# Kernel tuning notes

Measured on AMD Instinct MI355X. Metric: run time of the kernel, lower is better.

## Reference

```python
import jax, jax.numpy as jnp
import numpy as np

N_NODES = 100000
N_EDGES = 1600000
FEAT_DIM = 128
EMBED_DIM = 32
N_CLASS_P1 = 17  # num_class + 1


def setup_inputs() -> dict:
    key = jax.random.key(0)
    ks = jax.random.split(key, 6)
    features = jax.random.normal(ks[0], (N_NODES, FEAT_DIM), dtype=jnp.float32)
    edges = jax.random.randint(ks[1], (N_EDGES, 2), 0, N_NODES, dtype=jnp.int64)
    weights = jax.random.uniform(ks[2], (N_EDGES,), dtype=jnp.float32)
    neighbours_sum = jax.random.uniform(ks[3], (N_NODES, 1), dtype=jnp.float32)
    W_embed = jax.random.normal(ks[4], (FEAT_DIM, EMBED_DIM), dtype=jnp.float32) / np.sqrt(FEAT_DIM)
    b_embed = jnp.zeros((EMBED_DIM,), dtype=jnp.float32)
    W_trans = jax.random.normal(ks[5], (2 * EMBED_DIM, N_CLASS_P1), dtype=jnp.float32) / np.sqrt(2 * EMBED_DIM)
    b_trans = jnp.zeros((N_CLASS_P1,), dtype=jnp.float32)
    return {
        "features": features, "edges": edges, "weights": weights,
        "neighbours_sum": neighbours_sum, "W_embed": W_embed, "b_embed": b_embed,
        "W_trans": W_trans, "b_trans": b_trans,
    }


def reference(features, edges, weights, neighbours_sum, W_embed, b_embed, W_trans, b_trans):
    num_nodes = features.shape[0]
    # node embedding: Linear(feature_dim -> num_dims)
    embed = features @ W_embed + b_embed               # [N, D]
    src_e = embed[edges[:, 0]]                         # [E, D] gather
    dst_e = embed[edges[:, 1]]                         # [E, D] gather
    # operator_sy1: [(src+dst)/2, (src-dst)^2]
    E_feat = jnp.concatenate([(src_e + dst_e) * 0.5, (src_e - dst_e) ** 2], axis=1)  # [E, 2D]
    poss_edge = jax.nn.softmax(E_feat @ W_trans + b_trans, axis=1)  # [E, C+1]
    # weighted scatter-add into nodes via edges[:,0]
    value = poss_edge * weights[:, None]
    recall_node = jax.ops.segment_sum(value, edges[:, 0], num_segments=num_nodes)  # [N, C+1]
    poss_node = recall_node / neighbours_sum
    return poss_node, poss_edge, recall_node
```

## Files before the change

kernel.cpp:

```cpp
#include <hip/hip_runtime.h>

#define NNODES 100000
#define NEDGES 1600000
#define FDIM 128
#define EDIM 32
#define NCLS 17
#define ROWU 16
#define BCAP 64
#define WPK (16 * NCLS)

typedef unsigned int u32;
typedef _Float16 h2 __attribute__((ext_vector_type(2)));

__device__ inline h2 bch(u32 x) { return __builtin_bit_cast(h2, x); }

__device__ inline float dot2acc(h2 a, u32 wbits, float acc) {
#if __has_builtin(__builtin_amdgcn_fdot2)
  return __builtin_amdgcn_fdot2(a, bch(wbits), acc, false);
#else
  h2 w = bch(wbits);
  acc = fmaf((float)a[0], (float)w[0], acc);
  return fmaf((float)a[1], (float)w[1], acc);
#endif
}

__global__ __launch_bounds__(256) void prep_kernel(
    const float* __restrict__ W_trans, u32* __restrict__ wpack)
{
  for (int x = threadIdx.x; x < 2 * WPK; x += 256) {
    int tab = x / WPK;
    int r   = x - tab * WPK;
    int k2  = r / NCLS, c = r - k2 * NCLS;
    int row0 = tab ? (EDIM + 2 * k2) : (2 * k2);
    float a = W_trans[row0 * NCLS + c];
    float b = W_trans[(row0 + 1) * NCLS + c];
    if (!tab) { a *= 0.5f; b *= 0.5f; }
    h2 p; p[0] = (_Float16)a; p[1] = (_Float16)b;
    wpack[x] = __builtin_bit_cast(u32, p);
  }
}

__global__ __launch_bounds__(64) void node_kernel(
    const float* __restrict__ features,
    const float* __restrict__ W_embed,
    const float* __restrict__ b_embed,
    u32* __restrict__ nodetab)
{
  int n = blockIdx.x * 64 + threadIdx.x;
  if (n >= NNODES) return;

  float acc[EDIM];
  #pragma unroll
  for (int c = 0; c < EDIM; ++c) acc[c] = b_embed[c];

  const float4* f4 = (const float4*)(features + (size_t)n * FDIM);
  for (int k4 = 0; k4 < FDIM / 4; ++k4) {
    float4 f = f4[k4];
    const float* w = W_embed + k4 * 4 * EDIM;
    #pragma unroll
    for (int c = 0; c < EDIM; ++c) {
      acc[c] = fmaf(f.x, w[c],            acc[c]);
      acc[c] = fmaf(f.y, w[EDIM + c],     acc[c]);
      acc[c] = fmaf(f.z, w[2 * EDIM + c], acc[c]);
      acc[c] = fmaf(f.w, w[3 * EDIM + c], acc[c]);
    }
  }

  u32 p[16];
  #pragma unroll
  for (int i = 0; i < 16; ++i) {
    h2 t; t[0] = (_Float16)acc[2 * i]; t[1] = (_Float16)acc[2 * i + 1];
    p[i] = __builtin_bit_cast(u32, t);
  }
  uint4* row = (uint4*)(nodetab + (size_t)n * ROWU);
  #pragma unroll
  for (int i = 0; i < 4; ++i)
    row[i] = make_uint4(p[4 * i], p[4 * i + 1], p[4 * i + 2], p[4 * i + 3]);
}

template <int FAST>
__global__ __launch_bounds__(256, 4) void edge_kernel4(
    const int*   __restrict__ edges,
    const float* __restrict__ weights,
    const u32*   __restrict__ wpack,
    const float* __restrict__ b_trans,
    const u32*   __restrict__ nodetab,
    float* __restrict__ poss_edge,
    u32*   __restrict__ cursor,
    u32*   __restrict__ bucket,
    float* __restrict__ recall)
{
  __shared__ float sOut[256 * NCLS];
  __shared__ int   sSrc[256];
  int tid = threadIdx.x;
  int e = blockIdx.x * 256 + tid;
  int2 ed = ((const int2*)edges)[e];
  int src = ed.x, dst = ed.y;

  const uint4* rs4 = (const uint4*)(nodetab + (size_t)src * ROWU);
  const uint4* rd4 = (const uint4*)(nodetab + (size_t)dst * ROWU);
  uint4 sq[4] = {rs4[0], rs4[1], rs4[2], rs4[3]};
  uint4 dq[4] = {rd4[0], rd4[1], rd4[2], rd4[3]};
  float w = weights[e];

  if (FAST) {
    u32 slot = atomicAdd(cursor + src, 1u);
    if (slot < BCAP)
      ((uint2*)bucket)[(size_t)src * BCAP + slot] =
          make_uint2((u32)e, __float_as_uint(w));
  }

  float lgt[NCLS];
  #pragma unroll
  for (int c = 0; c < NCLS; ++c) lgt[c] = b_trans[c];

  #pragma unroll
  for (int q = 0; q < 4; ++q) {
    u32 su[4] = {sq[q].x, sq[q].y, sq[q].z, sq[q].w};
    u32 du[4] = {dq[q].x, dq[q].y, dq[q].z, dq[q].w};
    #pragma unroll
    for (int j = 0; j < 4; ++j) {
      int k2 = q * 4 + j;
      h2 s2 = bch(su[j]), d2 = bch(du[j]);
      h2 uu = s2 + d2;
      h2 t  = s2 - d2;
      h2 vv = t * t;
      const u32* w1 = wpack + k2 * NCLS;
      const u32* w2 = wpack + WPK + k2 * NCLS;
      #pragma unroll
      for (int c = 0; c < NCLS; ++c) {
        lgt[c] = dot2acc(uu, w1[c], lgt[c]);
        lgt[c] = dot2acc(vv, w2[c], lgt[c]);
      }
    }
  }

  float m = lgt[0];
  #pragma unroll
  for (int c = 1; c < NCLS; ++c) m = fmaxf(m, lgt[c]);
  float sum = 0.f;
  #pragma unroll
  for (int c = 0; c < NCLS; ++c) { lgt[c] = __expf(lgt[c] - m); sum += lgt[c]; }
  float inv = 1.0f / sum;

  #pragma unroll
  for (int c = 0; c < NCLS; ++c) sOut[tid * NCLS + c] = lgt[c] * inv;
  __syncthreads();

  float4* outp = (float4*)(poss_edge + (size_t)blockIdx.x * 256 * NCLS);
  const float4* sOut4 = (const float4*)sOut;
  for (int i = tid; i < 256 * NCLS / 4; i += 256)
    outp[i] = sOut4[i];

  if (!FAST) {
    __syncthreads();
    float wi = w * inv;
    sSrc[tid] = src;
    #pragma unroll
    for (int c = 0; c < NCLS; ++c) sOut[tid * NCLS + c] = lgt[c] * wi;
    __syncthreads();
    for (int i = tid; i < 256 * NCLS; i += 256) {
      unsigned e2 = (unsigned)i / NCLS;
      unsigned c2 = (unsigned)i - e2 * NCLS;
      atomicAdd(recall + (size_t)sSrc[e2] * NCLS + c2, sOut[i]);
    }
  }
}

__global__ __launch_bounds__(256, 8) void reduce_kernel(
    const float* __restrict__ poss_edge,
    const u32*   __restrict__ cursor,
    const u32*   __restrict__ bucket,
    const float* __restrict__ nsum,
    float* __restrict__ recall,
    float* __restrict__ poss_node)
{
  int tid = threadIdx.x;
  if (tid >= 255) return;
  int g = tid / 17;
  int n = blockIdx.x * 15 + g;
  if (n >= NNODES) return;
  int c = tid - g * 17;

  u32 deg = min(cursor[n], (u32)BCAP);
  float ns = nsum[n];
  const uint2* bk = (const uint2*)bucket + (size_t)n * BCAP;

  float acc = 0.f;
  u32 k = 0;
  for (; k + 4 <= deg; k += 4) {
    uint2 b0 = bk[k], b1 = bk[k + 1], b2 = bk[k + 2], b3 = bk[k + 3];
    float p0 = poss_edge[(size_t)b0.x * NCLS + c];
    float p1 = poss_edge[(size_t)b1.x * NCLS + c];
    float p2 = poss_edge[(size_t)b2.x * NCLS + c];
    float p3 = poss_edge[(size_t)b3.x * NCLS + c];
    acc = fmaf(p0, __uint_as_float(b0.y), acc);
    acc = fmaf(p1, __uint_as_float(b1.y), acc);
    acc = fmaf(p2, __uint_as_float(b2.y), acc);
    acc = fmaf(p3, __uint_as_float(b3.y), acc);
  }
  for (; k < deg; ++k) {
    uint2 b = bk[k];
    acc = fmaf(poss_edge[(size_t)b.x * NCLS + c], __uint_as_float(b.y), acc);
  }

  size_t o = (size_t)n * NCLS + c;
  recall[o]    = acc;
  poss_node[o] = acc / ns;
}

__global__ __launch_bounds__(256) void div_kernel(
    const float* __restrict__ recall,
    const float* __restrict__ nsum,
    float* __restrict__ poss_node)
{
  int i = blockIdx.x * 256 + threadIdx.x;
  if (i < NNODES * NCLS)
    poss_node[i] = recall[i] / nsum[i / NCLS];
}

extern "C" void kernel_launch(void* const* d_in, const int* in_sizes, int n_in,
                              void* d_out, int out_size, void* d_ws, size_t ws_size,
                              hipStream_t stream) {
  const float* features = (const float*)d_in[0];
  const int*   edges    = (const int*)d_in[1];
  const float* weights  = (const float*)d_in[2];
  const float* nsum     = (const float*)d_in[3];
  const float* W_embed  = (const float*)d_in[4];
  const float* b_embed  = (const float*)d_in[5];
  const float* W_trans  = (const float*)d_in[6];
  const float* b_trans  = (const float*)d_in[7];

  float* out       = (float*)d_out;
  float* poss_node = out;
  float* poss_edge = out + (size_t)NNODES * NCLS;
  float* recall    = out + (size_t)(NNODES + NEDGES) * NCLS;

  u32* nodetab = (u32*)d_ws;
  u32* cursor  = nodetab + (size_t)NNODES * ROWU;
  u32* wpack   = cursor + NNODES;
  u32* bucket  = wpack + 2 * WPK;
  size_t need_fast = ((size_t)NNODES * ROWU + NNODES + 2 * WPK
                     + (size_t)NNODES * BCAP * 2) * 4;
  size_t need_min  = ((size_t)NNODES * ROWU + NNODES + 2 * WPK) * 4;

  if (ws_size >= need_fast) {
    hipMemsetAsync(cursor, 0, (size_t)NNODES * sizeof(u32), stream);
    prep_kernel<<<1, 256, 0, stream>>>(W_trans, wpack);
    node_kernel<<<(NNODES + 63) / 64, 64, 0, stream>>>(features, W_embed, b_embed,
                                                       nodetab);
    edge_kernel4<1><<<NEDGES / 256, 256, 0, stream>>>(edges, weights, wpack, b_trans,
                                                      nodetab, poss_edge, cursor, bucket,
                                                      nullptr);
    reduce_kernel<<<(NNODES + 14) / 15, 256, 0, stream>>>(poss_edge, cursor, bucket,
                                                          nsum, recall, poss_node);
  } else if (ws_size >= need_min) {
    hipMemsetAsync(recall, 0, (size_t)NNODES * NCLS * sizeof(float), stream);
    prep_kernel<<<1, 256, 0, stream>>>(W_trans, wpack);
    node_kernel<<<(NNODES + 63) / 64, 64, 0, stream>>>(features, W_embed, b_embed,
                                                       nodetab);
    edge_kernel4<0><<<NEDGES / 256, 256, 0, stream>>>(edges, weights, wpack, b_trans,
                                                      nodetab, poss_edge, nullptr, nullptr,
                                                      recall);
    div_kernel<<<(NNODES * NCLS + 255) / 256, 256, 0, stream>>>(recall, nsum, poss_node);
  }
}
```

Baseline: 372.7 us.

## Replace fixed-capacity per-node buckets with exact CSR via histogram and prefix scan

Adds a histogram kernel over edge sources and a three-stage prefix scan to build exact CSR offsets. The edge kernel then writes (edge, weight) pairs into a compact CSR array, and the reduce kernel reads from it. This removes the 64-slot bucket cap that could drop edges and shrinks the workspace (1.6M entries instead of 6.4M). The cost is four extra small kernel launches and an extra pass over the edges for the histogram.

```diff
diff --git a/kernel.cpp b/kernel.cpp
--- a/kernel.cpp
+++ b/kernel.cpp
@@ -6,8 +6,9 @@
 #define EDIM 32
 #define NCLS 17
 #define ROWU 16
-#define BCAP 64
 #define WPK (16 * NCLS)
+#define SCB 1024
+#define NSB ((NNODES + SCB - 1) / SCB)
 
 typedef unsigned int u32;
 typedef _Float16 h2 __attribute__((ext_vector_type(2)));
@@ -37,6 +38,56 @@
     if (!tab) { a *= 0.5f; b *= 0.5f; }
     h2 p; p[0] = (_Float16)a; p[1] = (_Float16)b;
     wpack[x] = __builtin_bit_cast(u32, p);
+  }
+}
+
+__global__ __launch_bounds__(256) void hist_kernel(
+    const int* __restrict__ edges, u32* __restrict__ cnt)
+{
+  int i = blockIdx.x * 256 + threadIdx.x;
+  int4 e2 = ((const int4*)edges)[i];
+  atomicAdd(cnt + e2.x, 1u);
+  atomicAdd(cnt + e2.z, 1u);
+}
+
+__global__ __launch_bounds__(SCB) void scan1_kernel(
+    const u32* __restrict__ cnt, u32* __restrict__ base, u32* __restrict__ btot)
+{
+  __shared__ u32 s[SCB];
+  int tid = threadIdx.x;
+  int idx = blockIdx.x * SCB + tid;
+  u32 v = (idx < NNODES) ? cnt[idx] : 0u;
+  s[tid] = v; __syncthreads();
+  for (int off = 1; off < SCB; off <<= 1) {
+    u32 t = (tid >= off) ? s[tid - off] : 0u; __syncthreads();
+    s[tid] += t; __syncthreads();
+  }
+  if (idx < NNODES) base[idx] = s[tid] - v;
+  if (tid == SCB - 1) btot[blockIdx.x] = s[tid];
+}
+
+__global__ __launch_bounds__(128) void scan2_kernel(
+    const u32* __restrict__ btot, u32* __restrict__ boff)
+{
+  __shared__ u32 s[128];
+  int tid = threadIdx.x;
+  u32 v = (tid < NSB) ? btot[tid] : 0u;
+  s[tid] = v; __syncthreads();
+  for (int off = 1; off < 128; off <<= 1) {
+    u32 t = (tid >= off) ? s[tid - off] : 0u; __syncthreads();
+    s[tid] += t; __syncthreads();
+  }
+  if (tid < NSB) boff[tid] = s[tid] - v;
+}
+
+__global__ __launch_bounds__(SCB) void scan3_kernel(
+    u32* __restrict__ base, const u32* __restrict__ boff, u32* __restrict__ pos)
+{
+  int idx = blockIdx.x * SCB + threadIdx.x;
+  if (idx < NNODES) {
+    u32 b = base[idx] + boff[blockIdx.x];
+    base[idx] = b;
+    pos[idx]  = b;
   }
 }
 
@@ -79,15 +130,15 @@
 }
 
 template <int FAST>
-__global__ __launch_bounds__(256, 4) void edge_kernel4(
+__global__ __launch_bounds__(256, 4) void edge_kernel6(
     const int*   __restrict__ edges,
     const float* __restrict__ weights,
     const u32*   __restrict__ wpack,
     const float* __restrict__ b_trans,
     const u32*   __restrict__ nodetab,
     float* __restrict__ poss_edge,
-    u32*   __restrict__ cursor,
-    u32*   __restrict__ bucket,
+    u32*   __restrict__ pos,
+    uint2* __restrict__ csr,
     float* __restrict__ recall)
 {
   __shared__ float sOut[256 * NCLS];
@@ -104,10 +155,8 @@
   float w = weights[e];
 
   if (FAST) {
-    u32 slot = atomicAdd(cursor + src, 1u);
-    if (slot < BCAP)
-      ((uint2*)bucket)[(size_t)src * BCAP + slot] =
-          make_uint2((u32)e, __float_as_uint(w));
+    u32 slot = atomicAdd(pos + src, 1u);
+    csr[slot] = make_uint2((u32)e, __float_as_uint(w));
   }
 
   float lgt[NCLS];
@@ -169,8 +218,9 @@
 
 __global__ __launch_bounds__(256, 8) void reduce_kernel(
     const float* __restrict__ poss_edge,
-    const u32*   __restrict__ cursor,
-    const u32*   __restrict__ bucket,
+    const u32*   __restrict__ cnt,
+    const u32*   __restrict__ base,
+    const uint2* __restrict__ csr,
     const float* __restrict__ nsum,
     float* __restrict__ recall,
     float* __restrict__ poss_node)
@@ -182,9 +232,9 @@
   if (n >= NNODES) return;
   int c = tid - g * 17;
 
-  u32 deg = min(cursor[n], (u32)BCAP);
+  u32 deg = cnt[n];
   float ns = nsum[n];
-  const uint2* bk = (const uint2*)bucket + (size_t)n * BCAP;
+  const uint2* bk = csr + base[n];
 
   float acc = 0.f;
   u32 k = 0;
@@ -237,29 +287,37 @@
   float* recall    = out + (size_t)(NNODES + NEDGES) * NCLS;
 
   u32* nodetab = (u32*)d_ws;
-  u32* cursor  = nodetab + (size_t)NNODES * ROWU;
-  u32* wpack   = cursor + NNODES;
-  u32* bucket  = wpack + 2 * WPK;
-  size_t need_fast = ((size_t)NNODES * ROWU + NNODES + 2 * WPK
-                     + (size_t)NNODES * BCAP * 2) * 4;
-  size_t need_min  = ((size_t)NNODES * ROWU + NNODES + 2 * WPK) * 4;
+  u32* wpack   = nodetab + (size_t)NNODES * ROWU;
+  u32* cnt     = wpack + 2 * WPK;
+  u32* base    = cnt + NNODES;
+  u32* pos     = base + NNODES;
+  u32* btot    = pos + NNODES;
+  u32* boff    = btot + 128;
+  u32* csrw    = boff + 128;
+  uint2* csr   = (uint2*)csrw;
+  size_t need_fast = ((size_t)(csrw - (u32*)d_ws) + (size_t)NEDGES * 2) * 4;
+  size_t need_min  = ((size_t)NNODES * ROWU + 2 * WPK) * 4;
 
   if (ws_size >= need_fast) {
-    hipMemsetAsync(cursor, 0, (size_t)NNODES * sizeof(u32), stream);
+    hipMemsetAsync(cnt, 0, (size_t)NNODES * sizeof(u32), stream);
     prep_kernel<<<1, 256, 0, stream>>>(W_trans, wpack);
+    hist_kernel<<<NEDGES / 512, 256, 0, stream>>>(edges, cnt);
+    scan1_kernel<<<NSB, SCB, 0, stream>>>(cnt, base, btot);
+    scan2_kernel<<<1, 128, 0, stream>>>(btot, boff);
+    scan3_kernel<<<NSB, SCB, 0, stream>>>(base, boff, pos);
     node_kernel<<<(NNODES + 63) / 64, 64, 0, stream>>>(features, W_embed, b_embed,
                                                        nodetab);
-    edge_kernel4<1><<<NEDGES / 256, 256, 0, stream>>>(edges, weights, wpack, b_trans,
-                                                      nodetab, poss_edge, cursor, bucket,
+    edge_kernel6<1><<<NEDGES / 256, 256, 0, stream>>>(edges, weights, wpack, b_trans,
+                                                      nodetab, poss_edge, pos, csr,
                                                       nullptr);
-    reduce_kernel<<<(NNODES + 14) / 15, 256, 0, stream>>>(poss_edge, cursor, bucket,
+    reduce_kernel<<<(NNODES + 14) / 15, 256, 0, stream>>>(poss_edge, cnt, base, csr,
                                                           nsum, recall, poss_node);
   } else if (ws_size >= need_min) {
     hipMemsetAsync(recall, 0, (size_t)NNODES * NCLS * sizeof(float), stream);
     prep_kernel<<<1, 256, 0, stream>>>(W_trans, wpack);
     node_kernel<<<(NNODES + 63) / 64, 64, 0, stream>>>(features, W_embed, b_embed,
                                                        nodetab);
-    edge_kernel4<0><<<NEDGES / 256, 256, 0, stream>>>(edges, weights, wpack, b_trans,
+    edge_kernel6<0><<<NEDGES / 256, 256, 0, stream>>>(edges, weights, wpack, b_trans,
                                                       nodetab, poss_edge, nullptr, nullptr,
                                                       recall);
     div_kernel<<<(NNODES * NCLS + 255) / 256, 256, 0, stream>>>(recall, nsum, poss_node);
```

New measurement: 427.0 us. 14.6% more time.
